# Optimization experiments

Measured on AMD Instinct MI355X. Metric: run time of the kernel, lower is better.

## Reference

```python
import jax, jax.numpy as jnp
import numpy as np

B, T, S, D = 8, 512, 512, 1024
NUM_HEADS = 16
REUSE_HEADS = 8
NEW_HEADS = NUM_HEADS - REUSE_HEADS
KEY_DIM = 64
VALUE_DIM = 64
PE_MAX = 512  # pe_max_seq_length


def setup_inputs() -> dict:
    key = jax.random.key(0)
    ks = jax.random.split(key, 12)
    s = 0.02
    return {
        "query": jax.random.normal(ks[0], (B, T, D), jnp.float32),
        "value": jax.random.normal(ks[1], (B, S, D), jnp.float32),
        # scores reused from a previous layer (already softmaxed there)
        "reuse_attention_scores": jax.random.uniform(ks[2], (B, REUSE_HEADS, T, S), jnp.float32),
        "Wq": jax.random.normal(ks[3], (D, NEW_HEADS, KEY_DIM), jnp.float32) * s,
        "bq": jnp.zeros((NEW_HEADS, KEY_DIM), jnp.float32),
        "Wk": jax.random.normal(ks[4], (D, NEW_HEADS, KEY_DIM), jnp.float32) * s,
        "bk": jnp.zeros((NEW_HEADS, KEY_DIM), jnp.float32),
        "Wv": jax.random.normal(ks[5], (D, NUM_HEADS, VALUE_DIM), jnp.float32) * s,
        "bv": jnp.zeros((NUM_HEADS, VALUE_DIM), jnp.float32),
        # relative position embeddings: [1, new_heads, 2*PE_MAX - 1]
        "pos_emb": jax.random.truncated_normal(ks[6], -2.0, 2.0, (1, NEW_HEADS, 2 * PE_MAX - 1), jnp.float32) * 0.2,
        # output denses: one for reused heads (no bias), one for new heads (bias)
        "Wo_reuse": jax.random.normal(ks[7], (REUSE_HEADS, VALUE_DIM, D), jnp.float32) * s,
        "Wo_new": jax.random.normal(ks[8], (NEW_HEADS, VALUE_DIM, D), jnp.float32) * s,
        "bo": jnp.zeros((D,), jnp.float32),
    }


def reference(query, value, reuse_attention_scores, Wq, bq, Wk, bk, Wv, bv,
              pos_emb, Wo_reuse, Wo_new, bo):
    # projections (EinsumDense abc,cde->abde + bias over last two dims)
    q = jnp.einsum("btd,dnh->btnh", query, Wq) + bq           # [B,T,Hn,kd]
    k = jnp.einsum("bsd,dnh->bsnh", value, Wk) + bk           # [B,S,Hn,kd]
    v = jnp.einsum("bsd,dnh->bsnh", value, Wv) + bv           # [B,S,H,vd]
    v_reuse, v_new = v[:, :, :REUSE_HEADS, :], v[:, :, REUSE_HEADS:, :]

    # new-head scores: scaled QK^T  (dot_product_equation 'aecd,abcd->acbe')
    q = q * (1.0 / np.sqrt(float(KEY_DIM)))
    new_scores = jnp.einsum("bsnh,btnh->bnts", k, q)          # [B,Hn,T,S]

    # relative position bias: index = clip(key_pos - query_pos + PE_MAX-1)
    rel = jnp.arange(S)[None, :] - jnp.arange(T)[:, None] + (PE_MAX - 1)
    rel = jnp.clip(rel, 0, 2 * PE_MAX - 2)                    # [T,S]
    bias = pos_emb[0][:, rel]                                 # [Hn,T,S]
    new_scores = jax.nn.softmax(new_scores + bias[None], axis=-1)

    # reused heads consume previous-layer scores directly (dropout=0)
    reuse_scores = reuse_attention_scores[:, :REUSE_HEADS]
    out_reuse = jnp.einsum("bnts,bsnh->btnh", reuse_scores, v_reuse)
    out_new = jnp.einsum("bnts,bsnh->btnh", new_scores, v_new)

    # separate output projections, summed; bias only on the new-heads dense
    out = (jnp.einsum("btnh,nhd->btd", out_reuse, Wo_reuse)
           + jnp.einsum("btnh,nhd->btd", out_new, Wo_new) + bo)
    return out
```

## Files before the change

### kernel.cpp

```cpp
#include <hip/hip_runtime.h>
#include <hip/hip_bf16.h>

typedef __bf16 bf16_t;
typedef __bf16 bf16x8 __attribute__((ext_vector_type(8)));
typedef float  f32x4  __attribute__((ext_vector_type(4)));

#define GLDS(gsrc, ldst)                                                              \
  __builtin_amdgcn_global_load_lds(                                                   \
      (const __attribute__((address_space(1))) unsigned int*)(gsrc),                  \
      (__attribute__((address_space(3))) unsigned int*)(ldst), 16, 0, 0)

struct TArgs {
  const float* src[5];
  bf16_t* dst[5];
  int C[5], Ct[5], off[5], blk0[6];
  float scale[5];
};
struct CTArgs {
  const float* qa; bf16_t* qd;
  const float* va; bf16_t* vd;
  TArgs ta;
};
__global__ void k_convtrans(CTArgs ca) {
  __shared__ float tile[32][33];
  const int bid = blockIdx.x;
  if (bid < 4096) {
    int i = bid * 256 + threadIdx.x;
    const float* s; bf16_t* d;
    if (i < 524288) { s = ca.qa; d = ca.qd; } else { s = ca.va; d = ca.vd; i -= 524288; }
    const float4* p = reinterpret_cast<const float4*>(s) + 2 * (long)i;
    float4 x = p[0], y = p[1];
    bf16x8 o;
    o[0] = (bf16_t)x.x; o[1] = (bf16_t)x.y; o[2] = (bf16_t)x.z; o[3] = (bf16_t)x.w;
    o[4] = (bf16_t)y.x; o[5] = (bf16_t)y.y; o[6] = (bf16_t)y.z; o[7] = (bf16_t)y.w;
    reinterpret_cast<bf16x8*>(d)[i] = o;
    return;
  }
  const TArgs& ta = ca.ta;
  const int tb = bid - 4096;
  int s = 0;
  while (tb >= ta.blk0[s + 1]) ++s;
  const int bi = tb - ta.blk0[s];
  const int Ct = ta.Ct[s];
  const int c0 = (bi % Ct) * 32, r0 = (bi / Ct) * 32;
  const int C = ta.C[s];
  const float* src = ta.src[s];
  const int lx = threadIdx.x & 31, ly = threadIdx.x >> 5;
  #pragma unroll
  for (int i = 0; i < 32; i += 8)
    tile[ly + i][lx] = src[(long)(r0 + ly + i) * C + (c0 + lx)];
  __syncthreads();
  const float sc = ta.scale[s];
  bf16_t* dst = ta.dst[s];
  const int off = ta.off[s];
  #pragma unroll
  for (int i = 0; i < 32; i += 8)
    dst[(long)(c0 + ly + i) * 1024 + off + (r0 + lx)] = (bf16_t)(tile[lx][ly + i] * sc);
}

struct ProjItem {
  const bf16_t* A; const bf16_t* B; bf16_t* C; const float* bias;
  float bscale; int ldc; int writeT;
};
struct ProjArgs { ProjItem it[3]; };

__global__ __launch_bounds__(256)
void k_gemm_proj(ProjArgs pa) {
  __shared__ char smem[32768];
  const int bid = blockIdx.x;
  const int z = bid < 128 ? 0 : (bid < 256 ? 1 : 2);
  const int local = bid - (z == 0 ? 0 : (z == 1 ? 128 : 256));
  const ProjItem it = pa.it[z];
  const int t = threadIdx.x, lane = t & 63, wid = t >> 6;
  const int wr = wid >> 1, wc = wid & 1;
  const int m0 = (local & 31) * 128, n0 = (local >> 5) * 128;
  const int lhi = lane >> 4, llo = lane & 15;

  const bf16_t* Ab = it.A + (long)m0 * 1024;
  const bf16_t* Bb = it.B + (long)n0 * 1024;

  const int e0 = t * 8,        r0s = e0 >> 5, c0s = e0 & 31;
  const int e1 = (256 + t) * 8, r1s = e1 >> 5, c1s = e1 & 31;

#define PSTAGE(k0_, bsel)                                                     \
  { bf16_t* bA = (bf16_t*)(smem + (bsel) * 16384);                            \
    bf16_t* bB = (bf16_t*)(smem + (bsel) * 16384 + 8192);                     \
    GLDS(Ab + (long)r0s * 1024 + (k0_) + c0s, bA + wid * 512);                \
    GLDS(Ab + (long)r1s * 1024 + (k0_) + c1s, bA + 2048 + wid * 512);         \
    GLDS(Bb + (long)r0s * 1024 + (k0_) + c0s, bB + wid * 512);                \
    GLDS(Bb + (long)r1s * 1024 + (k0_) + c1s, bB + 2048 + wid * 512); }

  f32x4 acc[4][4] = {};
  PSTAGE(0, 0);
  __syncthreads();
  int cur = 0;
  for (int t32 = 0; t32 < 32; ++t32) {
    bf16_t* sA = (bf16_t*)(smem + cur * 16384);
    bf16_t* sB = (bf16_t*)(smem + cur * 16384 + 8192);
    bf16x8 a[4], b[4];
    #pragma unroll
    for (int mi = 0; mi < 4; ++mi)
      a[mi] = *reinterpret_cast<const bf16x8*>(sA + (wr * 64 + mi * 16 + llo) * 32 + lhi * 8);
    #pragma unroll
    for (int ni = 0; ni < 4; ++ni)
      b[ni] = *reinterpret_cast<const bf16x8*>(sB + (wc * 64 + ni * 16 + llo) * 32 + lhi * 8);
    if (t32 < 31) PSTAGE((t32 + 1) * 32, cur ^ 1);
    #pragma unroll
    for (int mi = 0; mi < 4; ++mi)
      #pragma unroll
      for (int ni = 0; ni < 4; ++ni)
        acc[mi][ni] = __builtin_amdgcn_mfma_f32_16x16x32_bf16(a[mi], b[ni], acc[mi][ni], 0, 0, 0);
    __syncthreads();
    cur ^= 1;
  }
#undef PSTAGE

  #pragma unroll
  for (int mi = 0; mi < 4; ++mi)
    #pragma unroll
    for (int ni = 0; ni < 4; ++ni) {
      const float bv = it.bias[n0 + wc * 64 + ni * 16 + llo] * it.bscale;
      #pragma unroll
      for (int r = 0; r < 4; ++r) acc[mi][ni][r] += bv;
    }

  if (!it.writeT) {
    bf16_t* E = (bf16_t*)smem;
    #pragma unroll
    for (int p = 0; p < 2; ++p) {
      if (wr == p) {
        #pragma unroll
        for (int mi = 0; mi < 4; ++mi)
          #pragma unroll
          for (int ni = 0; ni < 4; ++ni)
            #pragma unroll
            for (int r = 0; r < 4; ++r)
              E[(mi * 16 + lhi * 4 + r) * 136 + wc * 64 + ni * 16 + llo] = (bf16_t)acc[mi][ni][r];
      }
      __syncthreads();
      #pragma unroll
      for (int round = 0; round < 4; ++round) {
        const int row = (t >> 4) + round * 16;
        const int l16 = t & 15;
        float4 v = *reinterpret_cast<const float4*>((char*)E + row * 272 + l16 * 16);
        *reinterpret_cast<float4*>(it.C + (long)(m0 + p * 64 + row) * it.ldc + n0 + l16 * 8) = v;
      }
      __syncthreads();
    }
  } else {
    bf16_t* E = (bf16_t*)smem;
    #pragma unroll
    for (int p = 0; p < 2; ++p) {
      if (wr == p) {
        #pragma unroll
        for (int mi = 0; mi < 4; ++mi)
          #pragma unroll
          for (int ni = 0; ni < 4; ++ni)
            #pragma unroll
            for (int r = 0; r < 4; ++r)
              E[(wc * 64 + ni * 16 + llo) * 72 + mi * 16 + lhi * 4 + r] = (bf16_t)acc[mi][ni][r];
      }
      __syncthreads();
      #pragma unroll
      for (int round = 0; round < 4; ++round) {
        const int nr = (t >> 3) + round * 32;
        const int l8 = t & 7;
        float4 v = *reinterpret_cast<const float4*>((char*)E + nr * 144 + l8 * 16);
        *reinterpret_cast<float4*>(it.C + (long)(n0 + nr) * it.ldc + m0 + p * 64 + l8 * 8) = v;
      }
      __syncthreads();
    }
  }
}

__global__ __launch_bounds__(256)
void k_gemm_out(const bf16_t* __restrict__ A_, const bf16_t* __restrict__ B_,
                float* __restrict__ C_, const float* __restrict__ bias) {
  __shared__ char smem[24576];
  const int t = threadIdx.x, lane = t & 63, wid = t >> 6;
  const int wr = wid >> 1, wc = wid & 1;
  const int m0 = blockIdx.x * 64, n0 = blockIdx.y * 128;
  const int lhi = lane >> 4, llo = lane & 15;

  const bf16_t* Ab = A_ + (long)m0 * 1024;
  const bf16_t* Bb = B_ + (long)n0 * 1024;

  const int e0 = t * 8,        r0s = e0 >> 5, c0s = e0 & 31;
  const int e1 = (256 + t) * 8, r1s = e1 >> 5, c1s = e1 & 31;

#define OSTAGE(k0_, bsel)                                                     \
  { bf16_t* bA = (bf16_t*)(smem + (bsel) * 12288);                            \
    bf16_t* bB = (bf16_t*)(smem + (bsel) * 12288 + 4096);                     \
    GLDS(Ab + (long)r0s * 1024 + (k0_) + c0s, bA + wid * 512);                \
    GLDS(Bb + (long)r0s * 1024 + (k0_) + c0s, bB + wid * 512);                \
    GLDS(Bb + (long)r1s * 1024 + (k0_) + c1s, bB + 2048 + wid * 512); }

  f32x4 acc[2][4] = {};
  OSTAGE(0, 0);
  __syncthreads();
  int cur = 0;
  for (int t32 = 0; t32 < 32; ++t32) {
    bf16_t* sA = (bf16_t*)(smem + cur * 12288);
    bf16_t* sB = (bf16_t*)(smem + cur * 12288 + 4096);
    bf16x8 a[2], b[4];
    #pragma unroll
    for (int mi = 0; mi < 2; ++mi)
      a[mi] = *reinterpret_cast<const bf16x8*>(sA + (wr * 32 + mi * 16 + llo) * 32 + lhi * 8);
    #pragma unroll
    for (int ni = 0; ni < 4; ++ni)
      b[ni] = *reinterpret_cast<const bf16x8*>(sB + (wc * 64 + ni * 16 + llo) * 32 + lhi * 8);
    if (t32 < 31) OSTAGE((t32 + 1) * 32, cur ^ 1);
    #pragma unroll
    for (int mi = 0; mi < 2; ++mi)
      #pragma unroll
      for (int ni = 0; ni < 4; ++ni)
        acc[mi][ni] = __builtin_amdgcn_mfma_f32_16x16x32_bf16(a[mi], b[ni], acc[mi][ni], 0, 0, 0);
    __syncthreads();
    cur ^= 1;
  }
#undef OSTAGE

  #pragma unroll
  for (int mi = 0; mi < 2; ++mi)
    #pragma unroll
    for (int ni = 0; ni < 4; ++ni) {
      const float bv = bias[n0 + wc * 64 + ni * 16 + llo];
      #pragma unroll
      for (int r = 0; r < 4; ++r) acc[mi][ni][r] += bv;
    }

  float* E = (float*)smem;
  #pragma unroll
  for (int p = 0; p < 2; ++p) {
    if (wr == p) {
      #pragma unroll
      for (int mi = 0; mi < 2; ++mi)
        #pragma unroll
        for (int ni = 0; ni < 4; ++ni)
          #pragma unroll
          for (int r = 0; r < 4; ++r)
            E[(mi * 16 + lhi * 4 + r) * 132 + wc * 64 + ni * 16 + llo] = acc[mi][ni][r];
    }
    __syncthreads();
    #pragma unroll
    for (int round = 0; round < 4; ++round) {
      const int row = (t >> 5) + round * 8;
      const int l32 = t & 31;
      float4 v = *reinterpret_cast<const float4*>((char*)E + row * 528 + l32 * 16);
      *reinterpret_cast<float4*>(C_ + (long)(m0 + p * 32 + row) * 1024 + n0 + l32 * 4) = v;
    }
    __syncthreads();
  }
}

__global__ __launch_bounds__(256, 3)
void k_attn_all(const bf16_t* __restrict__ qb, const bf16_t* __restrict__ kb,
                const bf16_t* __restrict__ vbT, const float* __restrict__ pe,
                const float* __restrict__ reuse, bf16_t* __restrict__ om) {
  __shared__ char smem[53248];
  const int bid = blockIdx.x;
  const int lane = threadIdx.x & 63, w = threadIdx.x >> 6;
  const int lhi = lane >> 4, llo = lane & 15;

  if (bid < 512) {
    float* pes = (float*)smem;
    char* KtB = smem + 4096;
    char* VtB = smem + 4096 + 16384;
    char* PtB = smem + 4096 + 32768 + w * 4096;

    const int tt = bid >> 6;
    const int bh = bid & 63;
    const int b = bh >> 3, h = bh & 7;
    const int t0w = tt * 64 + w * 16;

    const bf16_t* Ksrc = kb + (long)(b * 512) * 512 + h * 64;
    const bf16_t* Vsrc = vbT + (long)(512 + h * 64) * 4096 + b * 512;
    const int krow = w * 32 + (lane >> 3);
    const int kcol = ((lane & 7) ^ (lane >> 3)) << 3;
    const int vn   = w * 16 + (lane >> 4);
    bf16_t* kdst = (bf16_t*)(KtB + w * 4096);
    bf16_t* vdst = (bf16_t*)(VtB + w * 4096);

#define STAGE_K(it_)                                                                   \
  { _Pragma("unroll")                                                                  \
    for (int g = 0; g < 4; ++g)                                                        \
      GLDS(Ksrc + (long)((it_) * 128 + krow + g * 8) * 512 + kcol, kdst + g * 512); }
#define STAGE_V(it_)                                                                   \
  { _Pragma("unroll")                                                                  \
    for (int g = 0; g < 4; ++g)                                                        \
      GLDS(Vsrc + (long)(vn + g * 4) * 4096 + (it_) * 128 +                            \
               (((lane & 15) ^ (g * 4 + (lane >> 4))) << 3),                           \
           vdst + g * 512); }

    STAGE_K(0);
    STAGE_V(0);

    const bf16_t* Qb = qb + (long)(b * 512 + t0w + llo) * 512 + h * 64;
    bf16x8 qf0 = *reinterpret_cast<const bf16x8*>(Qb + lhi * 8);
    bf16x8 qf1 = *reinterpret_cast<const bf16x8*>(Qb + 32 + lhi * 8);
    for (int i = threadIdx.x; i < 1023; i += 256) pes[i] = pe[h * 1023 + i];

    f32x4 oacc[4] = {};
    float lr[4] = {0.f, 0.f, 0.f, 0.f};

    __syncthreads();

    for (int it = 0; it < 4; ++it) {
      const int s0 = it * 128;

      f32x4 acc[8] = {};
      #pragma unroll
      for (int st = 0; st < 8; ++st) {
        const int rowb = st * 16 + llo;
        const int sw = (rowb & 7) << 4;
        bf16x8 kf0 = *reinterpret_cast<const bf16x8*>(KtB + rowb * 128 + ((lhi * 16) ^ sw));
        bf16x8 kf1 = *reinterpret_cast<const bf16x8*>(KtB + rowb * 128 + ((64 + lhi * 16) ^ sw));
        acc[st] = __builtin_amdgcn_mfma_f32_16x16x32_bf16(qf0, kf0, acc[st], 0, 0, 0);
        acc[st] = __builtin_amdgcn_mfma_f32_16x16x32_bf16(qf1, kf1, acc[st], 0, 0, 0);
      }

      __syncthreads();
      if (it < 3) STAGE_K(it + 1);

      #pragma unroll
      for (int r = 0; r < 4; ++r) {
        const int tl = lhi * 4 + r;
        const int bidx = s0 + llo - (t0w + tl) + 511;
        const int swp = (tl & 15) << 4;
        float lp = 0.f;
        #pragma unroll
        for (int st = 0; st < 8; ++st) {
          const float e = __expf(acc[st][r] + pes[bidx + st * 16]);
          lp += e;
          *reinterpret_cast<bf16_t*>(PtB + tl * 256 + (((st * 16 + llo) * 2) ^ swp)) = (bf16_t)e;
        }
        lr[r] += lp;
      }

      const int swa = llo << 4;
      #pragma unroll
      for (int ks = 0; ks < 4; ++ks) {
        bf16x8 pav = *reinterpret_cast<const bf16x8*>(PtB + llo * 256 + ((ks * 64 + lhi * 16) ^ swa));
        #pragma unroll
        for (int ni = 0; ni < 4; ++ni) {
          const int rowv = ni * 16 + llo;
          bf16x8 vf = *reinterpret_cast<const bf16x8*>(VtB + rowv * 256 + ((ks * 64 + lhi * 16) ^ swa));
          oacc[ni] = __builtin_amdgcn_mfma_f32_16x16x32_bf16(pav, vf, oacc[ni], 0, 0, 0);
        }
      }

      __syncthreads();
      if (it < 3) STAGE_V(it + 1);
    }

    #pragma unroll
    for (int r = 0; r < 4; ++r) {
      lr[r] += __shfl_xor(lr[r], 1);
      lr[r] += __shfl_xor(lr[r], 2);
      lr[r] += __shfl_xor(lr[r], 4);
      lr[r] += __shfl_xor(lr[r], 8);
    }

    bf16_t* Ew = (bf16_t*)PtB;
    #pragma unroll
    for (int ni = 0; ni < 4; ++ni)
      #pragma unroll
      for (int r = 0; r < 4; ++r)
        Ew[(lhi * 4 + r) * 72 + ni * 16 + llo] = (bf16_t)(oacc[ni][r] * (1.f / lr[r]));
    #pragma unroll
    for (int round = 0; round < 2; ++round) {
      const int lr8 = (lane >> 3) + round * 8;
      const int l8 = lane & 7;
      float4 v = *reinterpret_cast<const float4*>((char*)Ew + lr8 * 144 + l8 * 16);
      *reinterpret_cast<float4*>(om + (long)(b * 512 + t0w + lr8) * 1024 + 512 + h * 64 + l8 * 8) = v;
    }
#undef STAGE_K
#undef STAGE_V
    return;
  }

  typedef float RedRow[32][68];
  RedRow* red = (RedRow*)smem;
  const int pid = bid - 512;
  const int bh = pid >> 4;
  const int b = bh >> 3, head = bh & 7;
  const int m0 = (pid & 15) * 32;
  const int ks0 = w * 128;

  const float*  Af = reuse + (long)b * 2097152 + (long)head * 262144;
  const bf16_t* Bp = vbT + (long)(head * 64) * 4096 + b * 512;

  f32x4 acc[2][4] = {};
  float4 Ax[2][2][2];
  bf16x8 Bx[2][4];

  #define PV_LOAD(kq, buf)                                                              \
    {                                                                                   \
      const int kk = ks0 + (kq) * 32 + lhi * 8;                                         \
      _Pragma("unroll")                                                                 \
      for (int mi = 0; mi < 2; ++mi) {                                                  \
        const float4* p = reinterpret_cast<const float4*>(Af + (long)(m0 + mi * 16 + llo) * 512 + kk); \
        Ax[buf][mi][0] = p[0];                                                          \
        Ax[buf][mi][1] = p[1];                                                          \
      }                                                                                 \
      _Pragma("unroll")                                                                 \
      for (int ni = 0; ni < 4; ++ni)                                                    \
        Bx[buf][ni] = *reinterpret_cast<const bf16x8*>(Bp + (long)(ni * 16 + llo) * 4096 + kk); \
    }

  PV_LOAD(0, 0);
  #pragma unroll
  for (int kq = 0; kq < 4; ++kq) {
    const int cb = kq & 1;
    if (kq < 3) {
      const int nb = (kq + 1) & 1;
      PV_LOAD(kq + 1, nb);
    }
    bf16x8 a[2];
    #pragma unroll
    for (int mi = 0; mi < 2; ++mi) {
      float4 x = Ax[cb][mi][0], y = Ax[cb][mi][1];
      bf16x8 tv;
      tv[0] = (bf16_t)x.x; tv[1] = (bf16_t)x.y; tv[2] = (bf16_t)x.z; tv[3] = (bf16_t)x.w;
      tv[4] = (bf16_t)y.x; tv[5] = (bf16_t)y.y; tv[6] = (bf16_t)y.z; tv[7] = (bf16_t)y.w;
      a[mi] = tv;
    }
    #pragma unroll
    for (int mi = 0; mi < 2; ++mi)
      #pragma unroll
      for (int ni = 0; ni < 4; ++ni)
        acc[mi][ni] = __builtin_amdgcn_mfma_f32_16x16x32_bf16(a[mi], Bx[cb][ni], acc[mi][ni], 0, 0, 0);
  }
  #undef PV_LOAD

  if (w >= 2) {
    #pragma unroll
    for (int mi = 0; mi < 2; ++mi)
      #pragma unroll
      for (int ni = 0; ni < 4; ++ni)
        #pragma unroll
        for (int r = 0; r < 4; ++r)
          red[w - 2][mi * 16 + lhi * 4 + r][ni * 16 + llo] = acc[mi][ni][r];
  }
  __syncthreads();
  if (w < 2) {
    #pragma unroll
    for (int mi = 0; mi < 2; ++mi)
      #pragma unroll
      for (int ni = 0; ni < 4; ++ni)
        #pragma unroll
        for (int r = 0; r < 4; ++r)
          acc[mi][ni][r] += red[w][mi * 16 + lhi * 4 + r][ni * 16 + llo];
  }
  __syncthreads();
  if (w == 1) {
    #pragma unroll
    for (int mi = 0; mi < 2; ++mi)
      #pragma unroll
      for (int ni = 0; ni < 4; ++ni)
        #pragma unroll
        for (int r = 0; r < 4; ++r)
          red[0][mi * 16 + lhi * 4 + r][ni * 16 + llo] = acc[mi][ni][r];
  }
  __syncthreads();
  if (w == 0) {
    bf16_t* E = (bf16_t*)&red[1][0][0];
    #pragma unroll
    for (int mi = 0; mi < 2; ++mi)
      #pragma unroll
      for (int ni = 0; ni < 4; ++ni)
        #pragma unroll
        for (int r = 0; r < 4; ++r) {
          const int mr = mi * 16 + lhi * 4 + r;
          const int nn = ni * 16 + llo;
          E[mr * 72 + nn] = (bf16_t)(acc[mi][ni][r] + red[0][mr][nn]);
        }
    bf16_t* Cb = om + (long)b * 524288 + head * 64;
    #pragma unroll
    for (int round = 0; round < 4; ++round) {
      const int row = (lane >> 3) + round * 8;
      const int l8 = lane & 7;
      float4 v = *reinterpret_cast<const float4*>((char*)E + row * 144 + l8 * 16);
      *reinterpret_cast<float4*>(Cb + (long)(m0 + row) * 1024 + l8 * 8) = v;
    }
  }
}

extern "C" void kernel_launch(void* const* d_in, const int* in_sizes, int n_in,
                              void* d_out, int out_size, void* d_ws, size_t ws_size,
                              hipStream_t stream) {
  const float* query = (const float*)d_in[0];
  const float* value = (const float*)d_in[1];
  const float* reuse = (const float*)d_in[2];
  const float* Wq    = (const float*)d_in[3];
  const float* bq    = (const float*)d_in[4];
  const float* Wk    = (const float*)d_in[5];
  const float* bk    = (const float*)d_in[6];
  const float* Wv    = (const float*)d_in[7];
  const float* bv    = (const float*)d_in[8];
  const float* pe    = (const float*)d_in[9];
  const float* WoR   = (const float*)d_in[10];
  const float* WoN   = (const float*)d_in[11];
  const float* bo    = (const float*)d_in[12];
  float* out = (float*)d_out;
  (void)in_sizes; (void)n_in; (void)out_size; (void)ws_size;

  char* w = (char*)d_ws;
  bf16_t* qx  = (bf16_t*)(w);
  bf16_t* vx  = (bf16_t*)(w + (8L  << 20));
  bf16_t* WqT = (bf16_t*)(w + (16L << 20));
  bf16_t* WkT = (bf16_t*)(w + (17L << 20));
  bf16_t* WvT = (bf16_t*)(w + (18L << 20));
  bf16_t* WoT = (bf16_t*)(w + (20L << 20));
  bf16_t* qb  = (bf16_t*)(w + (22L << 20));
  bf16_t* kb  = (bf16_t*)(w + (26L << 20));
  bf16_t* vbT = (bf16_t*)(w + (30L << 20));
  bf16_t* om  = (bf16_t*)(w + (38L << 20));

  CTArgs ca;
  ca.qa = query; ca.qd = qx; ca.va = value; ca.vd = vx;
  ca.ta.src[0] = Wq;  ca.ta.dst[0] = WqT; ca.ta.C[0] = 512;  ca.ta.Ct[0] = 16; ca.ta.off[0] = 0;   ca.ta.scale[0] = 0.125f;
  ca.ta.src[1] = Wk;  ca.ta.dst[1] = WkT; ca.ta.C[1] = 512;  ca.ta.Ct[1] = 16; ca.ta.off[1] = 0;   ca.ta.scale[1] = 1.f;
  ca.ta.src[2] = Wv;  ca.ta.dst[2] = WvT; ca.ta.C[2] = 1024; ca.ta.Ct[2] = 32; ca.ta.off[2] = 0;   ca.ta.scale[2] = 1.f;
  ca.ta.src[3] = WoR; ca.ta.dst[3] = WoT; ca.ta.C[3] = 1024; ca.ta.Ct[3] = 32; ca.ta.off[3] = 0;   ca.ta.scale[3] = 1.f;
  ca.ta.src[4] = WoN; ca.ta.dst[4] = WoT; ca.ta.C[4] = 1024; ca.ta.Ct[4] = 32; ca.ta.off[4] = 512; ca.ta.scale[4] = 1.f;
  ca.ta.blk0[0] = 0; ca.ta.blk0[1] = 512; ca.ta.blk0[2] = 1024; ca.ta.blk0[3] = 2048; ca.ta.blk0[4] = 2560; ca.ta.blk0[5] = 3072;
  k_convtrans<<<dim3(7168), 256, 0, stream>>>(ca);

  ProjArgs pa;
  pa.it[0] = { qx, WqT, qb,  bq, 0.125f, 512,  0 };
  pa.it[1] = { vx, WkT, kb,  bk, 1.f,    512,  0 };
  pa.it[2] = { vx, WvT, vbT, bv, 1.f,    4096, 1 };
  k_gemm_proj<<<dim3(512), 256, 0, stream>>>(pa);

  k_attn_all<<<dim3(1536), 256, 0, stream>>>(qb, kb, vbT, pe, reuse, om);

  k_gemm_out<<<dim3(64, 8), 256, 0, stream>>>(om, WoT, out, bo);
}
```

Baseline: 90.53 us.

## Interleave attention and reuse-PV blocks; stage reuse scores through LDS with N-split waves

The block index is now interleaved so every third block runs a new-head attention tile and the other two run reuse-score PV tiles, which mixes compute-bound and bandwidth-bound work across CUs. The reuse PV path stops splitting K across waves with an LDS reduction. Instead it splits the 64 output columns across waves and double-buffers the fp32 score tile into swizzled LDS with global_load_lds, so each score element is fetched once per block and shared by all waves. This drops the multi-stage reduction and its barriers, but adds a barrier per K step and more LDS traffic for the fp32-to-bf16 conversion.

```diff
diff --git a/kernel.cpp b/kernel.cpp
--- a/kernel.cpp
+++ b/kernel.cpp
@@ -259,17 +259,21 @@
                 const float* __restrict__ reuse, bf16_t* __restrict__ om) {
   __shared__ char smem[53248];
   const int bid = blockIdx.x;
+  const int r3 = bid % 3;
+  const int q3 = bid / 3;
   const int lane = threadIdx.x & 63, w = threadIdx.x >> 6;
   const int lhi = lane >> 4, llo = lane & 15;
-
-  if (bid < 512) {
+  const int t = threadIdx.x;
+
+  if (r3 == 0) {
+    const int fidx = q3;
     float* pes = (float*)smem;
     char* KtB = smem + 4096;
     char* VtB = smem + 4096 + 16384;
     char* PtB = smem + 4096 + 32768 + w * 4096;
 
-    const int tt = bid >> 6;
-    const int bh = bid & 63;
+    const int tt = fidx >> 6;
+    const int bh = fidx & 63;
     const int b = bh >> 3, h = bh & 7;
     const int t0w = tt * 64 + w * 16;
 
@@ -298,7 +302,7 @@
     const bf16_t* Qb = qb + (long)(b * 512 + t0w + llo) * 512 + h * 64;
     bf16x8 qf0 = *reinterpret_cast<const bf16x8*>(Qb + lhi * 8);
     bf16x8 qf1 = *reinterpret_cast<const bf16x8*>(Qb + 32 + lhi * 8);
-    for (int i = threadIdx.x; i < 1023; i += 256) pes[i] = pe[h * 1023 + i];
+    for (int i = t; i < 1023; i += 256) pes[i] = pe[h * 1023 + i];
 
     f32x4 oacc[4] = {};
     float lr[4] = {0.f, 0.f, 0.f, 0.f};
@@ -379,110 +383,65 @@
     return;
   }
 
-  typedef float RedRow[32][68];
-  RedRow* red = (RedRow*)smem;
-  const int pid = bid - 512;
-  const int bh = pid >> 4;
+  const int pidx = q3 * 2 + (r3 - 1);
+  const int bh = pidx & 63;
+  const int mt = pidx >> 6;
   const int b = bh >> 3, head = bh & 7;
-  const int m0 = (pid & 15) * 32;
-  const int ks0 = w * 128;
-
-  const float*  Af = reuse + (long)b * 2097152 + (long)head * 262144;
-  const bf16_t* Bp = vbT + (long)(head * 64) * 4096 + b * 512;
-
-  f32x4 acc[2][4] = {};
-  float4 Ax[2][2][2];
-  bf16x8 Bx[2][4];
-
-  #define PV_LOAD(kq, buf)                                                              \
-    {                                                                                   \
-      const int kk = ks0 + (kq) * 32 + lhi * 8;                                         \
-      _Pragma("unroll")                                                                 \
-      for (int mi = 0; mi < 2; ++mi) {                                                  \
-        const float4* p = reinterpret_cast<const float4*>(Af + (long)(m0 + mi * 16 + llo) * 512 + kk); \
-        Ax[buf][mi][0] = p[0];                                                          \
-        Ax[buf][mi][1] = p[1];                                                          \
-      }                                                                                 \
-      _Pragma("unroll")                                                                 \
-      for (int ni = 0; ni < 4; ++ni)                                                    \
-        Bx[buf][ni] = *reinterpret_cast<const bf16x8*>(Bp + (long)(ni * 16 + llo) * 4096 + kk); \
-    }
-
-  PV_LOAD(0, 0);
-  #pragma unroll
-  for (int kq = 0; kq < 4; ++kq) {
-    const int cb = kq & 1;
-    if (kq < 3) {
-      const int nb = (kq + 1) & 1;
-      PV_LOAD(kq + 1, nb);
-    }
-    bf16x8 a[2];
-    #pragma unroll
-    for (int mi = 0; mi < 2; ++mi) {
-      float4 x = Ax[cb][mi][0], y = Ax[cb][mi][1];
-      bf16x8 tv;
-      tv[0] = (bf16_t)x.x; tv[1] = (bf16_t)x.y; tv[2] = (bf16_t)x.z; tv[3] = (bf16_t)x.w;
-      tv[4] = (bf16_t)y.x; tv[5] = (bf16_t)y.y; tv[6] = (bf16_t)y.z; tv[7] = (bf16_t)y.w;
-      a[mi] = tv;
-    }
-    #pragma unroll
-    for (int mi = 0; mi < 2; ++mi)
-      #pragma unroll
-      for (int ni = 0; ni < 4; ++ni)
-        acc[mi][ni] = __builtin_amdgcn_mfma_f32_16x16x32_bf16(a[mi], Bx[cb][ni], acc[mi][ni], 0, 0, 0);
-  }
-  #undef PV_LOAD
-
-  if (w >= 2) {
-    #pragma unroll
-    for (int mi = 0; mi < 2; ++mi)
-      #pragma unroll
-      for (int ni = 0; ni < 4; ++ni)
-        #pragma unroll
-        for (int r = 0; r < 4; ++r)
-          red[w - 2][mi * 16 + lhi * 4 + r][ni * 16 + llo] = acc[mi][ni][r];
-  }
+  const int m0 = mt * 32;
+  const int wc = w;
+
+  const float* Asrc = reuse + (long)b * 2097152 + (long)head * 262144 + (long)m0 * 512;
+  const bf16_t* Bp = vbT + (long)(head * 64 + wc * 16) * 4096 + b * 512;
+
+  const int arow = w * 2 + (lane >> 5);
+  const int acb  = (lane & 31) * 16;
+  const int asrcb = acb ^ ((arow & 7) << 5);
+  char* adst = smem + w * 1024 + (lane & 31) * 0;
+
+#define STAGE_A(ss_, bsel)                                                             \
+  { _Pragma("unroll")                                                                  \
+    for (int c = 0; c < 4; ++c)                                                        \
+      GLDS((const char*)(Asrc + (long)(c * 8 + arow) * 512 + (ss_) * 128) + asrcb,     \
+           smem + (bsel) * 16384 + c * 4096 + w * 1024); }
+
+  f32x4 acc[2] = {};
+  STAGE_A(0, 0);
   __syncthreads();
-  if (w < 2) {
-    #pragma unroll
-    for (int mi = 0; mi < 2; ++mi)
-      #pragma unroll
-      for (int ni = 0; ni < 4; ++ni)
-        #pragma unroll
-        for (int r = 0; r < 4; ++r)
-          acc[mi][ni][r] += red[w][mi * 16 + lhi * 4 + r][ni * 16 + llo];
-  }
+  int cur = 0;
+  for (int ss = 0; ss < 4; ++ss) {
+    if (ss < 3) STAGE_A(ss + 1, cur ^ 1);
+    const char* As = smem + cur * 16384;
+    #pragma unroll
+    for (int ks = 0; ks < 4; ++ks) {
+      bf16x8 bfrag = *reinterpret_cast<const bf16x8*>(Bp + (long)llo * 4096 + ss * 128 + ks * 32 + lhi * 8);
+      #pragma unroll
+      for (int mi = 0; mi < 2; ++mi) {
+        const int row = mi * 16 + llo;
+        const char* ap = As + row * 512 + ((ks * 128 + lhi * 32) ^ ((row & 7) << 5));
+        float4 x = *reinterpret_cast<const float4*>(ap);
+        float4 y = *reinterpret_cast<const float4*>(ap + 16);
+        bf16x8 av;
+        av[0] = (bf16_t)x.x; av[1] = (bf16_t)x.y; av[2] = (bf16_t)x.z; av[3] = (bf16_t)x.w;
+        av[4] = (bf16_t)y.x; av[5] = (bf16_t)y.y; av[6] = (bf16_t)y.z; av[7] = (bf16_t)y.w;
+        acc[mi] = __builtin_amdgcn_mfma_f32_16x16x32_bf16(av, bfrag, acc[mi], 0, 0, 0);
+      }
+    }
+    __syncthreads();
+    cur ^= 1;
+  }
+#undef STAGE_A
+
+  bf16_t* E = (bf16_t*)smem;
+  #pragma unroll
+  for (int mi = 0; mi < 2; ++mi)
+    #pragma unroll
+    for (int r = 0; r < 4; ++r)
+      E[(mi * 16 + lhi * 4 + r) * 72 + wc * 16 + llo] = (bf16_t)acc[mi][r];
   __syncthreads();
-  if (w == 1) {
-    #pragma unroll
-    for (int mi = 0; mi < 2; ++mi)
-      #pragma unroll
-      for (int ni = 0; ni < 4; ++ni)
-        #pragma unroll
-        for (int r = 0; r < 4; ++r)
-          red[0][mi * 16 + lhi * 4 + r][ni * 16 + llo] = acc[mi][ni][r];
-  }
-  __syncthreads();
-  if (w == 0) {
-    bf16_t* E = (bf16_t*)&red[1][0][0];
-    #pragma unroll
-    for (int mi = 0; mi < 2; ++mi)
-      #pragma unroll
-      for (int ni = 0; ni < 4; ++ni)
-        #pragma unroll
-        for (int r = 0; r < 4; ++r) {
-          const int mr = mi * 16 + lhi * 4 + r;
-          const int nn = ni * 16 + llo;
-          E[mr * 72 + nn] = (bf16_t)(acc[mi][ni][r] + red[0][mr][nn]);
-        }
-    bf16_t* Cb = om + (long)b * 524288 + head * 64;
-    #pragma unroll
-    for (int round = 0; round < 4; ++round) {
-      const int row = (lane >> 3) + round * 8;
-      const int l8 = lane & 7;
-      float4 v = *reinterpret_cast<const float4*>((char*)E + row * 144 + l8 * 16);
-      *reinterpret_cast<float4*>(Cb + (long)(m0 + row) * 1024 + l8 * 8) = v;
-    }
+  {
+    const int row = t >> 3, l8 = t & 7;
+    float4 v = *reinterpret_cast<const float4*>((char*)E + row * 144 + l8 * 16);
+    *reinterpret_cast<float4*>(om + (long)b * 524288 + (long)(m0 + row) * 1024 + head * 64 + l8 * 8) = v;
   }
 }
 
```

Result: slower. 102.6 us (+13.3%).

## Halve attention key tile, shrink LDS, interleave new and reuse blocks

Applied to the files above, without the earlier changes.

The flash-attention branch now processes 64 keys per iteration instead of 128, across 8 iterations. This cuts shared memory from 53KB to 28KB and raises the launch-bounds occupancy target from 3 to 5 blocks. Block indices are also remapped so that every third block runs the new-head attention path and the other two run the reuse-score PV path, which mixes compute-bound and memory-bound work on each CU. In exchange there are more iterations and barriers per block, plus modulo arithmetic in the block indexing. The epilogue scratch buffer is moved to the freed K/V region because the per-wave P buffer became too small.

```diff
diff --git a/kernel.cpp b/kernel.cpp
--- a/kernel.cpp
+++ b/kernel.cpp
@@ -253,44 +253,44 @@
   }
 }
 
-__global__ __launch_bounds__(256, 3)
+__global__ __launch_bounds__(256, 5)
 void k_attn_all(const bf16_t* __restrict__ qb, const bf16_t* __restrict__ kb,
                 const bf16_t* __restrict__ vbT, const float* __restrict__ pe,
                 const float* __restrict__ reuse, bf16_t* __restrict__ om) {
-  __shared__ char smem[53248];
+  __shared__ char smem[28672];
   const int bid = blockIdx.x;
+  const int r3 = bid % 3;
+  const int q3 = bid / 3;
   const int lane = threadIdx.x & 63, w = threadIdx.x >> 6;
   const int lhi = lane >> 4, llo = lane & 15;
 
-  if (bid < 512) {
+  if (r3 == 0) {
     float* pes = (float*)smem;
     char* KtB = smem + 4096;
-    char* VtB = smem + 4096 + 16384;
-    char* PtB = smem + 4096 + 32768 + w * 4096;
-
-    const int tt = bid >> 6;
-    const int bh = bid & 63;
+    char* VtB = smem + 12288;
+    char* PtB = smem + 20480 + w * 2048;
+
+    const int fidx = q3;
+    const int tt = fidx >> 6;
+    const int bh = fidx & 63;
     const int b = bh >> 3, h = bh & 7;
     const int t0w = tt * 64 + w * 16;
 
     const bf16_t* Ksrc = kb + (long)(b * 512) * 512 + h * 64;
     const bf16_t* Vsrc = vbT + (long)(512 + h * 64) * 4096 + b * 512;
-    const int krow = w * 32 + (lane >> 3);
+    const int krow = w * 16 + (lane >> 3);
     const int kcol = ((lane & 7) ^ (lane >> 3)) << 3;
-    const int vn   = w * 16 + (lane >> 4);
-    bf16_t* kdst = (bf16_t*)(KtB + w * 4096);
-    bf16_t* vdst = (bf16_t*)(VtB + w * 4096);
+    bf16_t* kdst = (bf16_t*)(KtB + w * 2048);
+    bf16_t* vdst = (bf16_t*)(VtB + w * 2048);
 
 #define STAGE_K(it_)                                                                   \
   { _Pragma("unroll")                                                                  \
-    for (int g = 0; g < 4; ++g)                                                        \
-      GLDS(Ksrc + (long)((it_) * 128 + krow + g * 8) * 512 + kcol, kdst + g * 512); }
+    for (int g = 0; g < 2; ++g)                                                        \
+      GLDS(Ksrc + (long)((it_) * 64 + krow + g * 8) * 512 + kcol, kdst + g * 512); }
 #define STAGE_V(it_)                                                                   \
   { _Pragma("unroll")                                                                  \
-    for (int g = 0; g < 4; ++g)                                                        \
-      GLDS(Vsrc + (long)(vn + g * 4) * 4096 + (it_) * 128 +                            \
-               (((lane & 15) ^ (g * 4 + (lane >> 4))) << 3),                           \
-           vdst + g * 512); }
+    for (int g = 0; g < 2; ++g)                                                        \
+      GLDS(Vsrc + (long)(krow + g * 8) * 4096 + (it_) * 64 + kcol, vdst + g * 512); }
 
     STAGE_K(0);
     STAGE_V(0);
@@ -305,12 +305,12 @@
 
     __syncthreads();
 
-    for (int it = 0; it < 4; ++it) {
-      const int s0 = it * 128;
-
-      f32x4 acc[8] = {};
-      #pragma unroll
-      for (int st = 0; st < 8; ++st) {
+    for (int it = 0; it < 8; ++it) {
+      const int s0 = it * 64;
+
+      f32x4 acc[4] = {};
+      #pragma unroll
+      for (int st = 0; st < 4; ++st) {
         const int rowb = st * 16 + llo;
         const int sw = (rowb & 7) << 4;
         bf16x8 kf0 = *reinterpret_cast<const bf16x8*>(KtB + rowb * 128 + ((lhi * 16) ^ sw));
@@ -320,37 +320,37 @@
       }
 
       __syncthreads();
-      if (it < 3) STAGE_K(it + 1);
+      if (it < 7) STAGE_K(it + 1);
 
       #pragma unroll
       for (int r = 0; r < 4; ++r) {
         const int tl = lhi * 4 + r;
         const int bidx = s0 + llo - (t0w + tl) + 511;
-        const int swp = (tl & 15) << 4;
+        const int swp = (tl & 7) << 4;
         float lp = 0.f;
         #pragma unroll
-        for (int st = 0; st < 8; ++st) {
+        for (int st = 0; st < 4; ++st) {
           const float e = __expf(acc[st][r] + pes[bidx + st * 16]);
           lp += e;
-          *reinterpret_cast<bf16_t*>(PtB + tl * 256 + (((st * 16 + llo) * 2) ^ swp)) = (bf16_t)e;
+          *reinterpret_cast<bf16_t*>(PtB + tl * 128 + (((st * 16 + llo) * 2) ^ swp)) = (bf16_t)e;
         }
         lr[r] += lp;
       }
 
-      const int swa = llo << 4;
-      #pragma unroll
-      for (int ks = 0; ks < 4; ++ks) {
-        bf16x8 pav = *reinterpret_cast<const bf16x8*>(PtB + llo * 256 + ((ks * 64 + lhi * 16) ^ swa));
+      const int swa = (llo & 7) << 4;
+      #pragma unroll
+      for (int ks = 0; ks < 2; ++ks) {
+        bf16x8 pav = *reinterpret_cast<const bf16x8*>(PtB + llo * 128 + ((ks * 64 + lhi * 16) ^ swa));
         #pragma unroll
         for (int ni = 0; ni < 4; ++ni) {
           const int rowv = ni * 16 + llo;
-          bf16x8 vf = *reinterpret_cast<const bf16x8*>(VtB + rowv * 256 + ((ks * 64 + lhi * 16) ^ swa));
+          bf16x8 vf = *reinterpret_cast<const bf16x8*>(VtB + rowv * 128 + ((ks * 64 + lhi * 16) ^ ((rowv & 7) << 4)));
           oacc[ni] = __builtin_amdgcn_mfma_f32_16x16x32_bf16(pav, vf, oacc[ni], 0, 0, 0);
         }
       }
 
       __syncthreads();
-      if (it < 3) STAGE_V(it + 1);
+      if (it < 7) STAGE_V(it + 1);
     }
 
     #pragma unroll
@@ -361,7 +361,7 @@
       lr[r] += __shfl_xor(lr[r], 8);
     }
 
-    bf16_t* Ew = (bf16_t*)PtB;
+    bf16_t* Ew = (bf16_t*)(smem + 4096 + w * 4096);
     #pragma unroll
     for (int ni = 0; ni < 4; ++ni)
       #pragma unroll
@@ -381,10 +381,11 @@
 
   typedef float RedRow[32][68];
   RedRow* red = (RedRow*)smem;
-  const int pid = bid - 512;
-  const int bh = pid >> 4;
+  const int pidx = q3 * 2 + (r3 - 1);
+  const int bh = pidx & 63;
+  const int mt = pidx >> 6;
   const int b = bh >> 3, head = bh & 7;
-  const int m0 = (pid & 15) * 32;
+  const int m0 = mt * 32;
   const int ks0 = w * 128;
 
   const float*  Af = reuse + (long)b * 2097152 + (long)head * 262144;
```

After: 89.28 us (median of 2 runs). About the same (-1.4%).
